# Kernel optimization log

Measured on AMD Instinct MI355X. Metric: run time of the kernel, lower is better.

The kernel has to match this reference:

```python
import jax, jax.numpy as jnp
import numpy as np

HIDDEN = 51
INPUT = 1
OUTPUT = 1
BATCH = 4096
SEQ = 999


def setup_inputs() -> dict:
    key = jax.random.key(0)
    ks = jax.random.split(key, 7)
    s = 1.0 / np.sqrt(HIDDEN)  # PyTorch default LSTM/Linear init scale
    u = lambda k, shape: jax.random.uniform(k, shape, jnp.float32, -s, s)
    return {
        "input": jax.random.normal(ks[0], (BATCH, SEQ, INPUT), jnp.float32),
        "W_ih": u(ks[1], (4 * HIDDEN, INPUT)),
        "W_hh": u(ks[2], (4 * HIDDEN, HIDDEN)),
        "b_ih": u(ks[3], (4 * HIDDEN,)),
        "b_hh": u(ks[4], (4 * HIDDEN,)),
        "W_fc": u(ks[5], (OUTPUT, HIDDEN)),
        "b_fc": u(ks[6], (OUTPUT,)),
        "future": 0,
    }


def reference(input, W_ih, W_hh, b_ih, b_hh, W_fc, b_fc, future):
    # Single-layer LSTM (PyTorch gate order i, f, g, o) scanned over time,
    # followed by a per-timestep Linear -> (batch, seq+future, output).
    def step(carry, x_t):
        h, c = carry
        gates = x_t @ W_ih.T + b_ih + h @ W_hh.T + b_hh  # (B, 4H)
        i, f, g, o = jnp.split(gates, 4, axis=-1)
        c = jax.nn.sigmoid(f) * c + jax.nn.sigmoid(i) * jnp.tanh(g)
        h = jax.nn.sigmoid(o) * jnp.tanh(c)
        return (h, c), h

    B = input.shape[0]
    h0 = jnp.zeros((B, HIDDEN), input.dtype)
    c0 = jnp.zeros((B, HIDDEN), input.dtype)
    xs = jnp.swapaxes(input, 0, 1)  # (T, B, I)
    (h, c), hs = jax.lax.scan(step, (h0, c0), xs)
    ys = hs @ W_fc.T + b_fc  # (T, B, O)

    # static Python int, so a trace-time loop is fine).
    y = ys[-1]
    extra = []
    for _ in range(future):
        (h, c), hn = step((h, c), y)
        y = hn @ W_fc.T + b_fc
        extra.append(y)
    if extra:
        ys = jnp.concatenate([ys, jnp.stack(extra, 0)], axis=0)
    return jnp.swapaxes(ys, 0, 1)  # (B, T+future, O)
```

## Files before the change

### kernel.cpp

```cpp
#include <hip/hip_runtime.h>
#include <hip/hip_bf16.h>

#define HID   51
#define MR    208
#define SEQT  999
#define CH    111
#define NCH   9
#define EPB   16
#define XST   17
#define NTH   832
#define BSTR  72

typedef __attribute__((ext_vector_type(8))) short  short8;
typedef __attribute__((ext_vector_type(4))) float  floatx4;

__global__ void prep_kernel(const float* __restrict__ W_hh,
                            const float* __restrict__ W_ih,
                            const float* __restrict__ W_fc,
                            __hip_bfloat16* __restrict__ A_ext)
{
    const float K1 = 1.442695040889f;
    int idx = blockIdx.x * blockDim.x + threadIdx.x;
    if (idx >= MR * 64) return;
    int r = idx >> 6, k = idx & 63;
    int u = r >> 2, gate = r & 3;
    float v = 0.f;
    if (r == 204) {
        if (k < HID) v = W_fc[k];
    } else if (u < HID) {
        float s = (gate == 2) ? (-2.f * K1) : (-K1);
        if (k < HID)      v = s * W_hh[(gate * HID + u) * HID + k];
        else if (k == 51) v = s * W_ih[gate * HID + u];
    }
    A_ext[idx] = __float2bfloat16(v);
}

__launch_bounds__(NTH)
__global__ void lstm_mfma_kernel(const float* __restrict__ x,
                                 const float* __restrict__ b_ih,
                                 const float* __restrict__ b_hh,
                                 const float* __restrict__ b_fc,
                                 const __hip_bfloat16* __restrict__ A_ext,
                                 float* __restrict__ out)
{
    __shared__ __hip_bfloat16 bcol[2][16 * BSTR];
    __shared__ float x_lds[(CH + 1) * XST];
    __shared__ float y_lds[CH * XST];

    const int tid  = threadIdx.x;
    const int w    = tid >> 6;
    const int lane = tid & 63;
    const int e    = lane & 15;
    const int g4   = lane >> 4;
    const int e0   = blockIdx.x * EPB;

    const int  u    = 4 * w + g4;
    const bool yln  = (u == 51);
    const bool xsv  = (w == 12) && (g4 == 0);
    const int  wrow = (u < HID) ? u : 63;

    const float K1  = 1.442695040889f;
    const float K2N = -2.885390081777f;

    short8  A0, A1;
    floatx4 bq = {0.f, 0.f, 0.f, 0.f};
    float   cs = 0.f;

    {
        int m = w * 16 + e;
        A0 = *(const short8*)&A_ext[m * 64 + g4 * 8];
        A1 = *(const short8*)&A_ext[m * 64 + 32 + g4 * 8];
    }
    if (u < HID) {
#pragma unroll
        for (int gg = 0; gg < 4; ++gg) {
            float s = (gg == 2) ? (-2.f * K1) : (-K1);
            bq[gg] = s * (b_ih[gg * HID + u] + b_hh[gg * HID + u]);
        }
    }

    for (int i = tid; i < 16 * BSTR; i += NTH) {
        bcol[0][i] = __float2bfloat16(0.f);
        bcol[1][i] = __float2bfloat16(0.f);
    }
    __syncthreads();
    if (tid < EPB)
        bcol[0][tid * BSTR + 51] = __float2bfloat16(x[(size_t)(e0 + tid) * SEQT]);
    const float bfc = b_fc[0];

    __syncthreads();

    for (int tc = 0; tc < NCH; ++tc) {
        const int t0 = tc * CH;
        for (int i2 = tid; i2 < (CH + 1) * EPB; i2 += NTH) {
            int ee = i2 / (CH + 1), tt = i2 % (CH + 1);
            int t = t0 + tt;
            x_lds[tt * XST + ee] = (t < SEQT) ? x[(size_t)(e0 + ee) * SEQT + t] : 0.f;
        }
        __syncthreads();

        for (int tt = 0; tt < CH; ++tt) {
            const int t  = t0 + tt;
            const int rp = t & 1, wp = rp ^ 1;

            short8 B0 = *(const short8*)&bcol[rp][e * BSTR + g4 * 8];
            short8 B1 = *(const short8*)&bcol[rp][e * BSTR + 32 + g4 * 8];

            floatx4 acc = __builtin_amdgcn_mfma_f32_16x16x32_bf16(A0, B0, bq, 0, 0, 0);
            acc = __builtin_amdgcn_mfma_f32_16x16x32_bf16(A1, B1, acc, 0, 0, 0);

            float Ei = __builtin_amdgcn_exp2f(acc[0]);
            float Ef = __builtin_amdgcn_exp2f(acc[1]);
            float Eg = __builtin_amdgcn_exp2f(acc[2]);
            float Eo = __builtin_amdgcn_exp2f(acc[3]);

            float P  = fmaf(Ei, Eg, (Ei + Eg) + 1.f);
            float F1 = 1.f + Ef;
            float R  = __builtin_amdgcn_rcpf(F1 * P);
            cs = fmaf(cs, P, K2N * ((1.f - Eg) * F1)) * R;

            float Ec  = __builtin_amdgcn_exp2f(cs);
            float Roc = __builtin_amdgcn_rcpf(fmaf(Eo, Ec, (Eo + Ec) + 1.f));
            float h   = (1.f - Ec) * Roc;

            bcol[wp][e * BSTR + wrow] = __float2bfloat16((u < HID) ? h : 0.f);
            if (yln) y_lds[tt * XST + e] = acc[0] + bfc;
            if (xsv) bcol[wp][e * BSTR + 51] =
                         __float2bfloat16(x_lds[(tt + 1) * XST + e]);

            __syncthreads();
        }
        __syncthreads();

        for (int i2 = tid; i2 < CH * EPB; i2 += NTH) {
            int ee = i2 / CH, tt = i2 % CH;
            int t = t0 + tt - 1;
            if (t >= 0)
                out[(size_t)(e0 + ee) * SEQT + t] = y_lds[tt * XST + ee];
        }
        __syncthreads();
    }

    if (w == 12) {
        short8 B0 = *(const short8*)&bcol[1][e * BSTR + g4 * 8];
        short8 B1 = *(const short8*)&bcol[1][e * BSTR + 32 + g4 * 8];
        floatx4 acc = __builtin_amdgcn_mfma_f32_16x16x32_bf16(A0, B0, bq, 0, 0, 0);
        acc = __builtin_amdgcn_mfma_f32_16x16x32_bf16(A1, B1, acc, 0, 0, 0);
        if (g4 == 3)
            out[(size_t)(e0 + e) * SEQT + (SEQT - 1)] = acc[0] + bfc;
    }
}

extern "C" void kernel_launch(void* const* d_in, const int* in_sizes, int n_in,
                              void* d_out, int out_size, void* d_ws, size_t ws_size,
                              hipStream_t stream) {
    const float* x    = (const float*)d_in[0];
    const float* W_ih = (const float*)d_in[1];
    const float* W_hh = (const float*)d_in[2];
    const float* b_ih = (const float*)d_in[3];
    const float* b_hh = (const float*)d_in[4];
    const float* W_fc = (const float*)d_in[5];
    const float* b_fc = (const float*)d_in[6];
    float* out = (float*)d_out;

    __hip_bfloat16* A_ext = (__hip_bfloat16*)d_ws;

    prep_kernel<<<(MR * 64 + 255) / 256, 256, 0, stream>>>(W_hh, W_ih, W_fc, A_ext);
    lstm_mfma_kernel<<<4096 / EPB, NTH, 0, stream>>>(x, b_ih, b_hh,
                                                     b_fc, A_ext, out);
}
```

Measured before the change: 498.5 us.

## Consolidate 13 waves into 4 waves each handling 3-4 MFMA tiles

```diff
diff --git a/kernel.cpp b/kernel.cpp
--- a/kernel.cpp
+++ b/kernel.cpp
@@ -8,7 +8,7 @@
 #define NCH   9
 #define EPB   16
 #define XST   17
-#define NTH   832
+#define NTH   256
 #define BSTR  72
 
 typedef __attribute__((ext_vector_type(8))) short  short8;
@@ -54,30 +54,40 @@
     const int g4   = lane >> 4;
     const int e0   = blockIdx.x * EPB;
 
-    const int  u    = 4 * w + g4;
-    const bool yln  = (u == 51);
-    const bool xsv  = (w == 12) && (g4 == 0);
-    const int  wrow = (u < HID) ? u : 63;
+    const int  NT  = (w == 3) ? 4 : 3;
+    const int  T0  = 3 * w;
+    const bool xsv = (w == 0) && (g4 == 0);
 
     const float K1  = 1.442695040889f;
     const float K2N = -2.885390081777f;
 
-    short8  A0, A1;
-    floatx4 bq = {0.f, 0.f, 0.f, 0.f};
-    float   cs = 0.f;
+    short8  A0[4], A1[4];
+    floatx4 bq[4];
+    float   cs[4] = {0.f, 0.f, 0.f, 0.f};
+    int     wr[4];
+    bool    real[4];
 
-    {
-        int m = w * 16 + e;
-        A0 = *(const short8*)&A_ext[m * 64 + g4 * 8];
-        A1 = *(const short8*)&A_ext[m * 64 + 32 + g4 * 8];
-    }
-    if (u < HID) {
 #pragma unroll
-        for (int gg = 0; gg < 4; ++gg) {
-            float s = (gg == 2) ? (-2.f * K1) : (-K1);
-            bq[gg] = s * (b_ih[gg * HID + u] + b_hh[gg * HID + u]);
+    for (int ti = 0; ti < 4; ++ti) {
+        bq[ti] = (floatx4){0.f, 0.f, 0.f, 0.f};
+        wr[ti] = 63; real[ti] = false;
+        if (ti < NT) {
+            int T = T0 + ti;
+            int m = T * 16 + e;
+            A0[ti] = *(const short8*)&A_ext[m * 64 + g4 * 8];
+            A1[ti] = *(const short8*)&A_ext[m * 64 + 32 + g4 * 8];
+            int u = 4 * T + g4;
+            if (u < HID) {
+                wr[ti] = u; real[ti] = true;
+#pragma unroll
+                for (int gg = 0; gg < 4; ++gg) {
+                    float s = (gg == 2) ? (-2.f * K1) : (-K1);
+                    bq[ti][gg] = s * (b_ih[gg * HID + u] + b_hh[gg * HID + u]);
+                }
+            }
         }
     }
+    const bool yln = (w == 3) && (g4 == 3);
 
     for (int i = tid; i < 16 * BSTR; i += NTH) {
         bcol[0][i] = __float2bfloat16(0.f);
@@ -106,25 +116,32 @@
             short8 B0 = *(const short8*)&bcol[rp][e * BSTR + g4 * 8];
             short8 B1 = *(const short8*)&bcol[rp][e * BSTR + 32 + g4 * 8];
 
-            floatx4 acc = __builtin_amdgcn_mfma_f32_16x16x32_bf16(A0, B0, bq, 0, 0, 0);
-            acc = __builtin_amdgcn_mfma_f32_16x16x32_bf16(A1, B1, acc, 0, 0, 0);
+#pragma unroll
+            for (int ti = 0; ti < 4; ++ti) {
+                if (ti >= NT) continue;
 
-            float Ei = __builtin_amdgcn_exp2f(acc[0]);
-            float Ef = __builtin_amdgcn_exp2f(acc[1]);
-            float Eg = __builtin_amdgcn_exp2f(acc[2]);
-            float Eo = __builtin_amdgcn_exp2f(acc[3]);
+                floatx4 acc = __builtin_amdgcn_mfma_f32_16x16x32_bf16(A0[ti], B0, bq[ti], 0, 0, 0);
+                acc = __builtin_amdgcn_mfma_f32_16x16x32_bf16(A1[ti], B1, acc, 0, 0, 0);
 
-            float P  = fmaf(Ei, Eg, (Ei + Eg) + 1.f);
-            float F1 = 1.f + Ef;
-            float R  = __builtin_amdgcn_rcpf(F1 * P);
-            cs = fmaf(cs, P, K2N * ((1.f - Eg) * F1)) * R;
+                float Ei = __builtin_amdgcn_exp2f(acc[0]);
+                float Ef = __builtin_amdgcn_exp2f(acc[1]);
+                float Eg = __builtin_amdgcn_exp2f(acc[2]);
+                float Eo = __builtin_amdgcn_exp2f(acc[3]);
 
-            float Ec  = __builtin_amdgcn_exp2f(cs);
-            float Roc = __builtin_amdgcn_rcpf(fmaf(Eo, Ec, (Eo + Ec) + 1.f));
-            float h   = (1.f - Ec) * Roc;
+                float P  = fmaf(Ei, Eg, (Ei + Eg) + 1.f);
+                float F1 = 1.f + Ef;
+                float R  = __builtin_amdgcn_rcpf(F1 * P);
+                cs[ti] = fmaf(cs[ti], P, K2N * ((1.f - Eg) * F1)) * R;
 
-            bcol[wp][e * BSTR + wrow] = __float2bfloat16((u < HID) ? h : 0.f);
-            if (yln) y_lds[tt * XST + e] = acc[0] + bfc;
+                float Ec  = __builtin_amdgcn_exp2f(cs[ti]);
+                float Roc = __builtin_amdgcn_rcpf(fmaf(Eo, Ec, (Eo + Ec) + 1.f));
+                float h   = (1.f - Ec) * Roc;
+
+                bcol[wp][e * BSTR + wr[ti]] = __float2bfloat16(real[ti] ? h : 0.f);
+                if (ti == 3 && yln)
+                    y_lds[tt * XST + e] = acc[0] + bfc;
+            }
+
             if (xsv) bcol[wp][e * BSTR + 51] =
                          __float2bfloat16(x_lds[(tt + 1) * XST + e]);
 
@@ -141,11 +158,11 @@
         __syncthreads();
     }
 
-    if (w == 12) {
+    if (w == 3) {
         short8 B0 = *(const short8*)&bcol[1][e * BSTR + g4 * 8];
         short8 B1 = *(const short8*)&bcol[1][e * BSTR + 32 + g4 * 8];
-        floatx4 acc = __builtin_amdgcn_mfma_f32_16x16x32_bf16(A0, B0, bq, 0, 0, 0);
-        acc = __builtin_amdgcn_mfma_f32_16x16x32_bf16(A1, B1, acc, 0, 0, 0);
+        floatx4 acc = __builtin_amdgcn_mfma_f32_16x16x32_bf16(A0[3], B0, bq[3], 0, 0, 0);
+        acc = __builtin_amdgcn_mfma_f32_16x16x32_bf16(A1[3], B1, acc, 0, 0, 0);
         if (g4 == 3)
             out[(size_t)(e0 + e) * SEQT + (SEQT - 1)] = acc[0] + bfc;
     }
```

After: 557.4 us. 1.12x slower.
